# Kernel tuning notes

Measured on AMD Instinct MI355X. Metric: run time of the kernel, lower is better.

Reference implementation:

```python
import jax, jax.numpy as jnp
import numpy as np

B, N, D, H = 16, 2048, 256, 256  # batch, sensor points, branch dim, hidden dim


def setup_inputs() -> dict:
    key = jax.random.key(0)
    ks = jax.random.split(key, 12)
    s = 0.02
    return {
        "x": jax.random.normal(ks[0], (B, N), dtype=jnp.float32),
        "grid": jax.random.uniform(ks[1], (N, 1), dtype=jnp.float32),  # cellcenters_nx
        "W1a": jax.random.normal(ks[2], (2, H), dtype=jnp.float32) * s,
        "b1a": jnp.zeros((H,), dtype=jnp.float32),
        "W1b": jax.random.normal(ks[3], (H, D), dtype=jnp.float32) * s,
        "b1b": jnp.zeros((D,), dtype=jnp.float32),
        "Wqkv": jax.random.normal(ks[4], (D, 3 * D), dtype=jnp.float32) * s,
        "W2a": jax.random.normal(ks[5], (D, H), dtype=jnp.float32) * s,
        "b2a": jnp.zeros((H,), dtype=jnp.float32),
        "W2b": jax.random.normal(ks[6], (H, D), dtype=jnp.float32) * s,
        "b2b": jnp.zeros((D,), dtype=jnp.float32),
    }


def reference(x, grid, W1a, b1a, W1b, b1b, Wqkv, W2a, b2a, W2b, b2b):
    b, n = x.shape
    # x.unsqueeze(-1) concat grid -> [B, N, 2]
    g = jnp.broadcast_to(grid[None, :, :], (b, n, 1))
    h = jnp.concatenate([x[..., None], g], axis=-1)
    # littleFNN Linear1: Linear -> GELU(exact) -> Linear
    h = jax.nn.gelu(h @ W1a + b1a, approximate=False) @ W1b + b1b  # [B, N, D]
    # SelfAttention: single fused qkv projection, no bias
    qkv = h @ Wqkv  # [B, N, 3D]
    q, k, v = jnp.split(qkv, 3, axis=-1)
    scale = jnp.asarray(qkv.shape[-1] // 3, h.dtype) ** -0.5
    scores = jnp.einsum("bid,bjd->bij", q, k) * scale  # [B, N, N]
    attn = jax.nn.softmax(scores, axis=-1)
    o = jnp.einsum("bij,bjd->bid", attn, v)  # [B, N, D]
    # littleFNN Linear2
    o = jax.nn.gelu(o @ W2a + b2a, approximate=False) @ W2b + b2b  # [B, N, D]
    return jnp.mean(o, axis=1)  # [B, D]
```

## Files before the change

### kernel.cpp

```cpp
#include <hip/hip_runtime.h>
#include <hip/hip_bf16.h>
#include <cmath>

typedef __attribute__((ext_vector_type(8))) short short8;
typedef __attribute__((ext_vector_type(4))) float f32x4;

#define MFMA16(a, b, c) __builtin_amdgcn_mfma_f32_16x16x32_bf16((a), (b), (c), 0, 0, 0)

static constexpr int BB = 16, NN = 2048, DD = 256, HH = 256;

__device__ inline unsigned short f2bf(float f) {
    union { float f; unsigned int u; } v; v.f = f;
    unsigned int r = v.u + 0x7fffu + ((v.u >> 16) & 1u);
    return (unsigned short)(r >> 16);
}
__device__ inline float bf2f(unsigned short u) {
    union { unsigned int u; float f; } v; v.u = ((unsigned int)u) << 16;
    return v.f;
}
__device__ inline float gelu_exact(float x) {
    return 0.5f * x * (1.0f + erff(x * 0.7071067811865475f));
}
__device__ inline void gload_lds16(const void* g, void* l) {
    __builtin_amdgcn_global_load_lds(
        (const __attribute__((address_space(1))) unsigned int*)g,
        (__attribute__((address_space(3))) unsigned int*)l, 16, 0, 0);
}
__device__ inline void fence_mem() { asm volatile("" ::: "memory"); }
__device__ inline unsigned int cvtpk_bf16(float lo, float hi) {
    unsigned int r;
    asm("v_cvt_pk_bf16_f32 %0, %1, %2" : "=v"(r) : "v"(lo), "v"(hi));
    return r;
}

__global__ __launch_bounds__(256) void transposeT_k(const float* __restrict__ W1b,
                                                    const float* __restrict__ Wqkv,
                                                    const float* __restrict__ W2a,
                                                    unsigned short* __restrict__ W1bT,
                                                    unsigned short* __restrict__ WqkvT,
                                                    unsigned short* __restrict__ W2aT,
                                                    float* __restrict__ bar) {
    __shared__ float tl[64][65];
    int bid = blockIdx.x;
    int t = threadIdx.x;
    if (bid == 0) {
        f32x4 z = (f32x4){0.f, 0.f, 0.f, 0.f};
#pragma unroll
        for (int i = 0; i < 4; i++) *(f32x4*)(bar + t * 16 + i * 4) = z;
    }
    const float* src;
    unsigned short* dst;
    int N, tn, tk;
    if (bid < 16) {
        src = W1b; dst = W1bT; N = 256; tn = bid & 3; tk = bid >> 2;
    } else if (bid < 64) {
        int t2 = bid - 16;
        src = Wqkv; dst = WqkvT; N = 768; tn = t2 % 12; tk = t2 / 12;
    } else {
        int t2 = bid - 64;
        src = W2a; dst = W2aT; N = 256; tn = t2 & 3; tk = t2 >> 2;
    }
    int n0 = tn * 64, k0 = tk * 64;
#pragma unroll
    for (int j = 0; j < 4; j++) {
        int row = (t >> 4) * 4 + j;
        f32x4 v = *(const f32x4*)(src + (size_t)(k0 + row) * N + n0 + (t & 15) * 4);
#pragma unroll
        for (int e = 0; e < 4; e++) tl[row][(t & 15) * 4 + e] = v[e];
    }
    __syncthreads();
    int n = t >> 2, cb = (t & 3) * 16;
    short8 a, b;
#pragma unroll
    for (int e = 0; e < 8; e++) {
        a[e] = (short)f2bf(tl[cb + e][n]);
        b[e] = (short)f2bf(tl[cb + 8 + e][n]);
    }
    *(short8*)(dst + (size_t)(n0 + n) * 256 + k0 + cb) = a;
    *(short8*)(dst + (size_t)(n0 + n) * 256 + k0 + cb + 8) = b;
}

__global__ __launch_bounds__(512) void ffn_qkv_k(const float* __restrict__ x,
                                                 const float* __restrict__ grd,
                                                 const float* __restrict__ W1a,
                                                 const float* __restrict__ b1a,
                                                 const unsigned short* __restrict__ W1bT,
                                                 const float* __restrict__ b1b,
                                                 const unsigned short* __restrict__ WqkvT,
                                                 unsigned short* __restrict__ qo,
                                                 unsigned short* __restrict__ ko,
                                                 unsigned short* __restrict__ vo) {
    __shared__ __attribute__((aligned(16))) char bstage[2][32768];
    __shared__ unsigned short h_lds[4][16 * 256];
    const int w = threadIdx.x >> 6, lane = threadIdx.x & 63;
    const int c = lane & 15, g = lane >> 4;
    const int qsub = w >> 1, nh = w & 1;
    const int rb = blockIdx.x * 64 + qsub * 16;
    const int bb = (blockIdx.x * 64) >> 11;
    const int rowinb = (rb & (NN - 1)) + c;

    const int p0r = rb + c;
    const float xv = x[p0r];
    const float gv = grd[p0r & (NN - 1)];
    short8 tf[8];
#pragma unroll
    for (int kc = 0; kc < 8; kc++) {
        int j0 = kc * 32 + g * 8;
#pragma unroll
        for (int e = 0; e < 8; e += 4) {
            f32x4 wa = *(const f32x4*)(W1a + j0 + e);
            f32x4 wb = *(const f32x4*)(W1a + 256 + j0 + e);
            f32x4 ba = *(const f32x4*)(b1a + j0 + e);
#pragma unroll
            for (int q = 0; q < 4; q++) {
                float v = xv * wa[q] + gv * wb[q] + ba[q];
                tf[kc][e + q] = (short)f2bf(gelu_exact(v));
            }
        }
    }

    const char* Bb0 = (const char*)W1bT;
    const char* Bb1 = (const char*)WqkvT;
    const char* Bb2 = (const char*)WqkvT + 256 * 512;
    const char* Bb3 = (const char*)WqkvT + 512 * 512;

#define STAGE_B(buf_, Bb_, kcp_) do {                                                    \
        _Pragma("unroll")                                                                \
        for (int i_ = 0; i_ < 4; i_++) {                                                 \
            int d_ = i_ * 8192 + w * 1024 + lane * 16;                                   \
            int row_ = d_ >> 7, sl_ = (d_ >> 4) & 7;                                     \
            gload_lds16(Bb_ + (size_t)row_ * 512 + (kcp_) * 128 +                        \
                            ((sl_ ^ (row_ & 7)) << 4),                                   \
                        &bstage[buf_][0] + d_);                                          \
        }                                                                                \
    } while (0)

    short8 hf[8];
#pragma unroll
    for (int kc = 0; kc < 8; kc++) hf[kc] = tf[kc];

    STAGE_B(0, Bb0, 0);

#pragma unroll
    for (int p = 0; p < 4; p++) {
        f32x4 acc[8];
#pragma unroll
        for (int n = 0; n < 8; n++) acc[n] = (f32x4){0.f, 0.f, 0.f, 0.f};

#pragma unroll
        for (int kcp = 0; kcp < 4; kcp++) {
            const int gi = p * 4 + kcp;
            if (gi + 1 < 16) {
                const int ni = gi + 1;
                const char* nb = (ni >> 2) == 0 ? Bb0 : (ni >> 2) == 1 ? Bb1
                                : (ni >> 2) == 2 ? Bb2 : Bb3;
                STAGE_B(ni & 1, nb, ni & 3);
                asm volatile("s_waitcnt vmcnt(4)" ::: "memory");
            } else {
                asm volatile("s_waitcnt vmcnt(0)" ::: "memory");
            }
            __builtin_amdgcn_s_barrier();
            fence_mem();

            const char* bl = &bstage[gi & 1][0];
#pragma unroll
            for (int sub = 0; sub < 2; sub++) {
                short8 a = (p == 0) ? tf[kcp * 2 + sub] : hf[kcp * 2 + sub];
#pragma unroll
                for (int n = 0; n < 8; n++) {
                    int addr = (nh * 128 + n * 16 + c) * 128 +
                               ((((sub << 2) | g) ^ (c & 7)) << 4);
                    short8 bfr = *(const short8*)(bl + addr);
                    if (p == 3) acc[n] = MFMA16(bfr, a, acc[n]);
                    else        acc[n] = MFMA16(a, bfr, acc[n]);
                }
            }
            fence_mem();
            __builtin_amdgcn_s_barrier();
            fence_mem();
        }

        if (p == 0) {
            unsigned short* hl = &h_lds[qsub][0];
#pragma unroll
            for (int n = 0; n < 8; n++) {
                int col = nh * 128 + n * 16 + c;
                float bv = b1b[col];
#pragma unroll
                for (int r = 0; r < 4; r++) {
                    int row = g * 4 + r;
                    hl[row * 256 + (col ^ ((row & 7) << 3))] = f2bf(acc[n][r] + bv);
                }
            }
            __syncthreads();
#pragma unroll
            for (int kc = 0; kc < 8; kc++) {
                hf[kc] = *(const short8*)(hl + c * 256 + ((kc * 32 + g * 8) ^ ((c & 7) << 3)));
            }
        } else if (p == 1) {
#pragma unroll
            for (int n = 0; n < 8; n++)
#pragma unroll
                for (int r = 0; r < 4; r++)
                    qo[(size_t)(rb + g * 4 + r) * 256 + nh * 128 + n * 16 + c] =
                        f2bf(acc[n][r] * (0.0625f * 1.4426950408889634f));
        } else if (p == 2) {
#pragma unroll
            for (int n = 0; n < 8; n++)
#pragma unroll
                for (int r = 0; r < 4; r++)
                    ko[(size_t)(rb + g * 4 + r) * 256 + nh * 128 + n * 16 + c] =
                        f2bf(acc[n][r]);
        } else {
#pragma unroll
            for (int m = 0; m < 8; m++) {
#pragma unroll
                for (int r = 0; r < 4; r++) {
                    int dcol = nh * 128 + m * 16 + g * 4 + r;
                    vo[((size_t)(bb * 256 + dcol)) * NN + rowinb] = f2bf(acc[m][r]);
                }
            }
        }
    }
#undef STAGE_B
}

__global__ __launch_bounds__(512) void attn_k(const unsigned short* __restrict__ qb,
                                              const unsigned short* __restrict__ kb,
                                              const unsigned short* __restrict__ vTb,
                                              const unsigned short* __restrict__ W2aT,
                                              const float* __restrict__ b2a,
                                              float* __restrict__ bar) {
    __shared__ __attribute__((aligned(16))) char smem[74752];
    char* klds = smem;
    char* vlds = smem + 32768;
    unsigned int* p_lds = (unsigned int*)(smem + 65536);
    float* exm = (float*)(smem + 65536 + 8192);
    float* exl = exm + 128;
    const int tid = threadIdx.x;
    const int w = tid >> 6, lane = tid & 63;
    const int c = lane & 15, g = lane >> 4;
    const int qsub = w & 3, dhalf = w >> 2;
    const int khalf = dhalf;
    const int bid = blockIdx.x;
    const int swz = (bid & 7) * 64 + (bid >> 3);
    const int b = swz >> 5;
    const int qt = swz & 31;
    const int qbase = qt * 64 + qsub * 16;
    constexpr int NT = NN / 64;

    const int sl_sub = lane >> 5;
    const int sl_col = (lane & 31) * 16;
    const int vl_row = lane >> 3;
    const size_t vl_off = (size_t)vl_row * (NN * 2) + (size_t)(((lane & 7) ^ vl_row) << 4);

    const short8* qp = (const short8*)(qb + (size_t)(b * NN + qbase + c) * DD + g * 8);
    short8 qf[8];
#pragma unroll
    for (int kc = 0; kc < 8; kc++) qf[kc] = qp[kc * 4];

    const char* kb_bytes = (const char*)(kb + (size_t)(b * NN) * DD);
    const char* vb_bytes = (const char*)(vTb + (size_t)(b * DD) * NN);
    const int kswz = (c & 7) << 4;
    const int pcs = c & 7;

#define STAGE_K(kt_) do {                                                                \
        const char* gk = kb_bytes + ((size_t)((kt_) * 64 + 8 * w)) * 512;                \
        _Pragma("unroll")                                                                \
        for (int s_ = 0; s_ < 4; s_++) {                                                 \
            int row_lo = 2 * s_ + sl_sub;                                                \
            gload_lds16(gk + (size_t)row_lo * 512 + (sl_col ^ (row_lo << 4)),            \
                        klds + (8 * w + 2 * s_) * 512);                                  \
        }                                                                                \
    } while (0)
#define STAGE_V(kt_) do {                                                                \
        const char* gv = vb_bytes + (size_t)(32 * w) * (NN * 2) + (size_t)(kt_) * 128 + vl_off; \
        _Pragma("unroll")                                                                \
        for (int s_ = 0; s_ < 4; s_++) {                                                 \
            gload_lds16(gv + (size_t)(8 * s_) * (NN * 2),                                \
                        vlds + (32 * w + 8 * s_) * 128);                                 \
        }                                                                                \
    } while (0)

    f32x4 oacc[8];
#pragma unroll
    for (int i = 0; i < 8; i++) oacc[i] = (f32x4){0.f, 0.f, 0.f, 0.f};
    float mrun = -INFINITY;
    float lrun = 0.f;
    unsigned int* plw = p_lds + qsub * 512 + c * 32;

    STAGE_K(0);

    for (int kt = 0; kt < NT; kt++) {
        STAGE_V(kt);
        asm volatile("s_waitcnt vmcnt(4)" ::: "memory");
        __builtin_amdgcn_s_barrier();
        fence_mem();

        const char* klb = klds + (size_t)(khalf * 32) * 512;
        f32x4 s0 = (f32x4){0.f, 0.f, 0.f, 0.f};
        f32x4 s1 = (f32x4){0.f, 0.f, 0.f, 0.f};
        __builtin_amdgcn_s_setprio(1);
#pragma unroll
        for (int kc = 0; kc < 8; kc++) {
            short8 qv = qf[kc];
            int col = (kc * 64 + g * 16) ^ kswz;
            short8 kf0 = *(const short8*)(klb + (size_t)c * 512 + col);
            short8 kf1 = *(const short8*)(klb + (size_t)(c + 16) * 512 + col);
            s0 = MFMA16(kf0, qv, s0);
            s1 = MFMA16(kf1, qv, s1);
        }
        __builtin_amdgcn_s_setprio(0);

        float t0 = fmaxf(fmaxf(s0[0], s0[1]), fmaxf(s0[2], s0[3]));
        float t1 = fmaxf(fmaxf(s1[0], s1[1]), fmaxf(s1[2], s1[3]));
        float tmo = fmaxf(t0, t1);
        tmo = fmaxf(tmo, __shfl_xor(tmo, 16));
        tmo = fmaxf(tmo, __shfl_xor(tmo, 32));
        if (g == 0) exm[w * 16 + c] = tmo;
        fence_mem();
        __builtin_amdgcn_s_barrier();
        fence_mem();
        float tmax = fmaxf(tmo, exm[(w ^ 4) * 16 + c]);

        if (kt + 1 < NT) STAGE_K(kt + 1);

        bool need = tmax > mrun + 8.f;
        if (__any(need)) {
            float mn = fmaxf(mrun, tmax);
            float corr = exp2f(mrun - mn);
#pragma unroll
            for (int r = 0; r < 4; r++) s0[r] = exp2f(s0[r] - mn);
#pragma unroll
            for (int r = 0; r < 4; r++) s1[r] = exp2f(s1[r] - mn);
            lrun = lrun * corr + ((s0[0] + s0[1]) + (s0[2] + s0[3])) +
                   ((s1[0] + s1[1]) + (s1[2] + s1[3]));
            mrun = mn;
#pragma unroll
            for (int r = 0; r < 4; r++) {
                float cr = __shfl(corr, 20 * g + r);
#pragma unroll
                for (int nc = 0; nc < 8; nc++) oacc[nc][r] *= cr;
            }
        } else {
#pragma unroll
            for (int r = 0; r < 4; r++) s0[r] = exp2f(s0[r] - mrun);
#pragma unroll
            for (int r = 0; r < 4; r++) s1[r] = exp2f(s1[r] - mrun);
            lrun += ((s0[0] + s0[1]) + (s0[2] + s0[3])) +
                    ((s1[0] + s1[1]) + (s1[2] + s1[3]));
        }

        {
            int jb0 = khalf * 16 + 2 * g;
            int jb1 = khalf * 16 + 8 + 2 * g;
#pragma unroll
            for (int h = 0; h < 2; h++) {
                int j = jb0 + h;
                plw[(((j >> 2) ^ pcs) << 2) | (j & 3)] = cvtpk_bf16(s0[2 * h], s0[2 * h + 1]);
                j = jb1 + h;
                plw[(((j >> 2) ^ pcs) << 2) | (j & 3)] = cvtpk_bf16(s1[2 * h], s1[2 * h + 1]);
            }
        }
        fence_mem();
        if (kt + 1 < NT) {
            asm volatile("s_waitcnt vmcnt(4)" ::: "memory");
        } else {
            asm volatile("s_waitcnt vmcnt(0)" ::: "memory");
        }
        __builtin_amdgcn_s_barrier();
        fence_mem();

        short8 pf0 = *(const short8*)(plw + ((g ^ pcs) << 2));
        short8 pf1 = *(const short8*)(plw + (((4 + g) ^ pcs) << 2));
        __builtin_amdgcn_s_setprio(1);
#pragma unroll
        for (int nc = 0; nc < 8; nc++) {
            const char* vr = vlds + (size_t)(dhalf * 128 + nc * 16 + c) * 128;
            short8 vf0 = *(const short8*)(vr + ((g ^ pcs) << 4));
            short8 vf1 = *(const short8*)(vr + (((4 + g) ^ pcs) << 4));
            oacc[nc] = MFMA16(pf0, vf0, oacc[nc]);
            oacc[nc] = MFMA16(pf1, vf1, oacc[nc]);
        }
        __builtin_amdgcn_s_setprio(0);

        fence_mem();
        __builtin_amdgcn_s_barrier();
        fence_mem();
    }
#undef STAGE_K
#undef STAGE_V

    float lt = lrun;
    lt += __shfl_xor(lt, 16);
    lt += __shfl_xor(lt, 32);
    if (g == 0) exl[w * 16 + c] = lt;
    fence_mem();
    __builtin_amdgcn_s_barrier();
    fence_mem();
    lt += exl[(w ^ 4) * 16 + c];
    float inv_r[4];
#pragma unroll
    for (int r = 0; r < 4; r++) inv_r[r] = 1.f / __shfl(lt, 20 * g + r);

    unsigned short* ol = (unsigned short*)smem;
#pragma unroll
    for (int r = 0; r < 4; r++) {
        int row = 4 * g + r;
        int swr = (row & 7) << 3;
#pragma unroll
        for (int nc = 0; nc < 8; nc++) {
            int col = dhalf * 128 + nc * 16 + c;
            ol[qsub * 4096 + row * 256 + (col ^ swr)] = f2bf(oacc[nc][r] * inv_r[r]);
        }
    }
    fence_mem();
    __builtin_amdgcn_s_barrier();
    fence_mem();

    {
        const int wcol = w * 32;
        float colsum[2] = {0.f, 0.f};
#pragma unroll
        for (int q2 = 0; q2 < 4; q2++) {
            f32x4 acc2[2];
            acc2[0] = (f32x4){0.f, 0.f, 0.f, 0.f};
            acc2[1] = (f32x4){0.f, 0.f, 0.f, 0.f};
            const unsigned short* oq = ol + q2 * 4096;
            const int swc = (c & 7) << 3;
#pragma unroll
            for (int kc = 0; kc < 8; kc++) {
                short8 a = *(const short8*)(oq + c * 256 + ((kc * 32 + g * 8) ^ swc));
#pragma unroll
                for (int nc = 0; nc < 2; nc++) {
                    short8 bfr = *(const short8*)(W2aT + (size_t)(wcol + nc * 16 + c) * 256 + kc * 32 + g * 8);
                    acc2[nc] = MFMA16(a, bfr, acc2[nc]);
                }
            }
#pragma unroll
            for (int nc = 0; nc < 2; nc++) {
                float bv = b2a[wcol + nc * 16 + c];
                float s2 = 0.f;
#pragma unroll
                for (int r = 0; r < 4; r++) s2 += gelu_exact(acc2[nc][r] + bv);
                colsum[nc] += s2;
            }
        }
#pragma unroll
        for (int nc = 0; nc < 2; nc++) {
            float s2 = colsum[nc];
            s2 += __shfl_xor(s2, 16);
            s2 += __shfl_xor(s2, 32);
            if (g == 0) atomicAdd(&bar[b * 256 + wcol + nc * 16 + c], s2);
        }
    }
}

__global__ void final_k(const float* __restrict__ bar, const float* __restrict__ W2b,
                        const float* __restrict__ b2b, float* __restrict__ out) {
    int b = blockIdx.x, d = threadIdx.x;
    float s = 0.f;
    for (int h = 0; h < HH; h++) s += bar[b * HH + h] * W2b[h * DD + d];
    out[b * DD + d] = b2b[d] + s * (1.f / (float)NN);
}

extern "C" void kernel_launch(void* const* d_in, const int* in_sizes, int n_in,
                              void* d_out, int out_size, void* d_ws, size_t ws_size,
                              hipStream_t stream) {
    (void)in_sizes; (void)n_in; (void)out_size; (void)ws_size;
    const float* x    = (const float*)d_in[0];
    const float* grd  = (const float*)d_in[1];
    const float* W1a  = (const float*)d_in[2];
    const float* b1a  = (const float*)d_in[3];
    const float* W1b  = (const float*)d_in[4];
    const float* b1b  = (const float*)d_in[5];
    const float* Wqkv = (const float*)d_in[6];
    const float* W2a  = (const float*)d_in[7];
    const float* b2a  = (const float*)d_in[8];
    const float* W2b  = (const float*)d_in[9];
    const float* b2b  = (const float*)d_in[10];
    float* out = (float*)d_out;

    char* ws = (char*)d_ws;
    const size_t MB = 1024 * 1024;
    unsigned short* q_buf  = (unsigned short*)(ws + 0);
    unsigned short* k_buf  = (unsigned short*)(ws + 16 * MB);
    unsigned short* vT_buf = (unsigned short*)(ws + 32 * MB);
    unsigned short* W1bT   = (unsigned short*)(ws + 80 * MB);
    unsigned short* WqkvT  = (unsigned short*)(ws + 80 * MB + 512 * 1024);
    unsigned short* W2aT   = (unsigned short*)(ws + 81 * MB);
    float*          bar    = (float*)(ws + 81 * MB + 256 * 1024);

    transposeT_k<<<dim3(80), 256, 0, stream>>>(W1b, Wqkv, W2a, W1bT, WqkvT, W2aT, bar);
    ffn_qkv_k<<<dim3(512), 512, 0, stream>>>(x, grd, W1a, b1a, W1bT, b1b, WqkvT,
                                             q_buf, k_buf, vT_buf);
    attn_k<<<dim3(512), 512, 0, stream>>>(q_buf, k_buf, vT_buf, W2aT, b2a, bar);
    final_k<<<dim3(BB), 256, 0, stream>>>(bar, W2b, b2b, out);
}
```

Before: 196.1 us.

## Halve attention tile to 32 queries x 32 keys with 4-wave blocks

Restructures the flash-attention kernel from 512-thread blocks handling 64 queries with 64-key tiles to 256-thread blocks handling 32 queries with 32-key tiles, doubling the grid to 1024 blocks. LDS use drops from about 73KB to about 35KB. This allows more resident blocks per CU and spreads the work over more blocks. In exchange, each K/V tile staged from global memory is reused by fewer queries, the loop runs twice as many iterations, and each iteration does fewer MFMAs between its barriers.

```diff
diff --git a/kernel.cpp b/kernel.cpp
--- a/kernel.cpp
+++ b/kernel.cpp
@@ -225,34 +225,34 @@
 #undef STAGE_B
 }
 
-__global__ __launch_bounds__(512) void attn_k(const unsigned short* __restrict__ qb,
+__global__ __launch_bounds__(256) void attn_k(const unsigned short* __restrict__ qb,
                                               const unsigned short* __restrict__ kb,
                                               const unsigned short* __restrict__ vTb,
                                               const unsigned short* __restrict__ W2aT,
                                               const float* __restrict__ b2a,
                                               float* __restrict__ bar) {
-    __shared__ __attribute__((aligned(16))) char smem[74752];
+    __shared__ __attribute__((aligned(16))) char smem[35328];
     char* klds = smem;
-    char* vlds = smem + 32768;
-    unsigned int* p_lds = (unsigned int*)(smem + 65536);
-    float* exm = (float*)(smem + 65536 + 8192);
-    float* exl = exm + 128;
+    char* vlds = smem + 16384;
+    unsigned int* p_lds = (unsigned int*)(smem + 32768);
+    float* exm = (float*)(smem + 34816);
+    float* exl = exm + 64;
     const int tid = threadIdx.x;
     const int w = tid >> 6, lane = tid & 63;
     const int c = lane & 15, g = lane >> 4;
-    const int qsub = w & 3, dhalf = w >> 2;
+    const int qsub = w & 1, dhalf = w >> 1;
     const int khalf = dhalf;
     const int bid = blockIdx.x;
-    const int swz = (bid & 7) * 64 + (bid >> 3);
-    const int b = swz >> 5;
-    const int qt = swz & 31;
-    const int qbase = qt * 64 + qsub * 16;
-    constexpr int NT = NN / 64;
+    const int swz = (bid & 7) * 128 + (bid >> 3);
+    const int b = swz >> 6;
+    const int qt = swz & 63;
+    const int qbase = qt * 32 + qsub * 16;
+    constexpr int NT = NN / 32;
 
     const int sl_sub = lane >> 5;
     const int sl_col = (lane & 31) * 16;
-    const int vl_row = lane >> 3;
-    const size_t vl_off = (size_t)vl_row * (NN * 2) + (size_t)(((lane & 7) ^ vl_row) << 4);
+    const int vl_row = lane >> 2;
+    const int vl_col = (((lane & 3) ^ (vl_row & 3)) << 4);
 
     const short8* qp = (const short8*)(qb + (size_t)(b * NN + qbase + c) * DD + g * 8);
     short8 qf[8];
@@ -262,10 +262,10 @@
     const char* kb_bytes = (const char*)(kb + (size_t)(b * NN) * DD);
     const char* vb_bytes = (const char*)(vTb + (size_t)(b * DD) * NN);
     const int kswz = (c & 7) << 4;
-    const int pcs = c & 7;
+    const int pcs = c & 3;
 
 #define STAGE_K(kt_) do {                                                                \
-        const char* gk = kb_bytes + ((size_t)((kt_) * 64 + 8 * w)) * 512;                \
+        const char* gk = kb_bytes + ((size_t)((kt_) * 32 + 8 * w)) * 512;                \
         _Pragma("unroll")                                                                \
         for (int s_ = 0; s_ < 4; s_++) {                                                 \
             int row_lo = 2 * s_ + sl_sub;                                                \
@@ -274,11 +274,12 @@
         }                                                                                \
     } while (0)
 #define STAGE_V(kt_) do {                                                                \
-        const char* gv = vb_bytes + (size_t)(32 * w) * (NN * 2) + (size_t)(kt_) * 128 + vl_off; \
+        const char* gv = vb_bytes + (size_t)(64 * w + vl_row) * (NN * 2) +               \
+                         (size_t)(kt_) * 64 + vl_col;                                    \
         _Pragma("unroll")                                                                \
         for (int s_ = 0; s_ < 4; s_++) {                                                 \
-            gload_lds16(gv + (size_t)(8 * s_) * (NN * 2),                                \
-                        vlds + (32 * w + 8 * s_) * 128);                                 \
+            gload_lds16(gv + (size_t)(16 * s_) * (NN * 2),                               \
+                        vlds + (4 * w + s_) * 1024);                                     \
         }                                                                                \
     } while (0)
 
@@ -287,7 +288,7 @@
     for (int i = 0; i < 8; i++) oacc[i] = (f32x4){0.f, 0.f, 0.f, 0.f};
     float mrun = -INFINITY;
     float lrun = 0.f;
-    unsigned int* plw = p_lds + qsub * 512 + c * 32;
+    unsigned int* plw = p_lds + qsub * 256 + c * 16;
 
     STAGE_K(0);
 
@@ -297,31 +298,24 @@
         __builtin_amdgcn_s_barrier();
         fence_mem();
 
-        const char* klb = klds + (size_t)(khalf * 32) * 512;
         f32x4 s0 = (f32x4){0.f, 0.f, 0.f, 0.f};
-        f32x4 s1 = (f32x4){0.f, 0.f, 0.f, 0.f};
         __builtin_amdgcn_s_setprio(1);
 #pragma unroll
         for (int kc = 0; kc < 8; kc++) {
-            short8 qv = qf[kc];
             int col = (kc * 64 + g * 16) ^ kswz;
-            short8 kf0 = *(const short8*)(klb + (size_t)c * 512 + col);
-            short8 kf1 = *(const short8*)(klb + (size_t)(c + 16) * 512 + col);
-            s0 = MFMA16(kf0, qv, s0);
-            s1 = MFMA16(kf1, qv, s1);
+            short8 kf = *(const short8*)(klds + (size_t)(khalf * 16 + c) * 512 + col);
+            s0 = MFMA16(kf, qf[kc], s0);
         }
         __builtin_amdgcn_s_setprio(0);
 
-        float t0 = fmaxf(fmaxf(s0[0], s0[1]), fmaxf(s0[2], s0[3]));
-        float t1 = fmaxf(fmaxf(s1[0], s1[1]), fmaxf(s1[2], s1[3]));
-        float tmo = fmaxf(t0, t1);
+        float tmo = fmaxf(fmaxf(s0[0], s0[1]), fmaxf(s0[2], s0[3]));
         tmo = fmaxf(tmo, __shfl_xor(tmo, 16));
         tmo = fmaxf(tmo, __shfl_xor(tmo, 32));
         if (g == 0) exm[w * 16 + c] = tmo;
         fence_mem();
         __builtin_amdgcn_s_barrier();
         fence_mem();
-        float tmax = fmaxf(tmo, exm[(w ^ 4) * 16 + c]);
+        float tmax = fmaxf(tmo, exm[(w ^ 2) * 16 + c]);
 
         if (kt + 1 < NT) STAGE_K(kt + 1);
 
@@ -331,10 +325,7 @@
             float corr = exp2f(mrun - mn);
 #pragma unroll
             for (int r = 0; r < 4; r++) s0[r] = exp2f(s0[r] - mn);
-#pragma unroll
-            for (int r = 0; r < 4; r++) s1[r] = exp2f(s1[r] - mn);
-            lrun = lrun * corr + ((s0[0] + s0[1]) + (s0[2] + s0[3])) +
-                   ((s1[0] + s1[1]) + (s1[2] + s1[3]));
+            lrun = lrun * corr + ((s0[0] + s0[1]) + (s0[2] + s0[3]));
             mrun = mn;
 #pragma unroll
             for (int r = 0; r < 4; r++) {
@@ -345,21 +336,15 @@
         } else {
 #pragma unroll
             for (int r = 0; r < 4; r++) s0[r] = exp2f(s0[r] - mrun);
-#pragma unroll
-            for (int r = 0; r < 4; r++) s1[r] = exp2f(s1[r] - mrun);
-            lrun += ((s0[0] + s0[1]) + (s0[2] + s0[3])) +
-                    ((s1[0] + s1[1]) + (s1[2] + s1[3]));
+            lrun += ((s0[0] + s0[1]) + (s0[2] + s0[3]));
         }
 
         {
-            int jb0 = khalf * 16 + 2 * g;
-            int jb1 = khalf * 16 + 8 + 2 * g;
+            int jb = khalf * 8 + 2 * g;
 #pragma unroll
             for (int h = 0; h < 2; h++) {
-                int j = jb0 + h;
+                int j = jb + h;
                 plw[(((j >> 2) ^ pcs) << 2) | (j & 3)] = cvtpk_bf16(s0[2 * h], s0[2 * h + 1]);
-                j = jb1 + h;
-                plw[(((j >> 2) ^ pcs) << 2) | (j & 3)] = cvtpk_bf16(s1[2 * h], s1[2 * h + 1]);
             }
         }
         fence_mem();
@@ -371,16 +356,13 @@
         __builtin_amdgcn_s_barrier();
         fence_mem();
 
-        short8 pf0 = *(const short8*)(plw + ((g ^ pcs) << 2));
-        short8 pf1 = *(const short8*)(plw + (((4 + g) ^ pcs) << 2));
+        short8 pf = *(const short8*)(plw + ((g ^ pcs) << 2));
         __builtin_amdgcn_s_setprio(1);
 #pragma unroll
         for (int nc = 0; nc < 8; nc++) {
-            const char* vr = vlds + (size_t)(dhalf * 128 + nc * 16 + c) * 128;
-            short8 vf0 = *(const short8*)(vr + ((g ^ pcs) << 4));
-            short8 vf1 = *(const short8*)(vr + (((4 + g) ^ pcs) << 4));
-            oacc[nc] = MFMA16(pf0, vf0, oacc[nc]);
-            oacc[nc] = MFMA16(pf1, vf1, oacc[nc]);
+            const char* vr = vlds + (size_t)(dhalf * 128 + nc * 16 + c) * 64;
+            short8 vf = *(const short8*)(vr + ((g ^ pcs) << 4));
+            oacc[nc] = MFMA16(pf, vf, oacc[nc]);
         }
         __builtin_amdgcn_s_setprio(0);
 
@@ -398,7 +380,7 @@
     fence_mem();
     __builtin_amdgcn_s_barrier();
     fence_mem();
-    lt += exl[(w ^ 4) * 16 + c];
+    lt += exl[(w ^ 2) * 16 + c];
     float inv_r[4];
 #pragma unroll
     for (int r = 0; r < 4; r++) inv_r[r] = 1.f / __shfl(lt, 20 * g + r);
@@ -411,7 +393,7 @@
 #pragma unroll
         for (int nc = 0; nc < 8; nc++) {
             int col = dhalf * 128 + nc * 16 + c;
-            ol[qsub * 4096 + row * 256 + (col ^ swr)] = f2bf(oacc[nc][r] * inv_r[r]);
+            ol[(qsub * 16 + row) * 256 + (col ^ swr)] = f2bf(oacc[nc][r] * inv_r[r]);
         }
     }
     fence_mem();
@@ -419,26 +401,26 @@
     fence_mem();
 
     {
-        const int wcol = w * 32;
-        float colsum[2] = {0.f, 0.f};
-#pragma unroll
-        for (int q2 = 0; q2 < 4; q2++) {
-            f32x4 acc2[2];
-            acc2[0] = (f32x4){0.f, 0.f, 0.f, 0.f};
-            acc2[1] = (f32x4){0.f, 0.f, 0.f, 0.f};
-            const unsigned short* oq = ol + q2 * 4096;
+        const int wcol = w * 64;
+        float colsum[4] = {0.f, 0.f, 0.f, 0.f};
+#pragma unroll
+        for (int q2 = 0; q2 < 2; q2++) {
+            f32x4 acc2[4];
+#pragma unroll
+            for (int nc = 0; nc < 4; nc++) acc2[nc] = (f32x4){0.f, 0.f, 0.f, 0.f};
+            const unsigned short* oq = ol + q2 * 16 * 256;
             const int swc = (c & 7) << 3;
 #pragma unroll
             for (int kc = 0; kc < 8; kc++) {
                 short8 a = *(const short8*)(oq + c * 256 + ((kc * 32 + g * 8) ^ swc));
 #pragma unroll
-                for (int nc = 0; nc < 2; nc++) {
+                for (int nc = 0; nc < 4; nc++) {
                     short8 bfr = *(const short8*)(W2aT + (size_t)(wcol + nc * 16 + c) * 256 + kc * 32 + g * 8);
                     acc2[nc] = MFMA16(a, bfr, acc2[nc]);
                 }
             }
 #pragma unroll
-            for (int nc = 0; nc < 2; nc++) {
+            for (int nc = 0; nc < 4; nc++) {
                 float bv = b2a[wcol + nc * 16 + c];
                 float s2 = 0.f;
 #pragma unroll
@@ -447,7 +429,7 @@
             }
         }
 #pragma unroll
-        for (int nc = 0; nc < 2; nc++) {
+        for (int nc = 0; nc < 4; nc++) {
             float s2 = colsum[nc];
             s2 += __shfl_xor(s2, 16);
             s2 += __shfl_xor(s2, 32);
@@ -494,6 +476,6 @@
     transposeT_k<<<dim3(80), 256, 0, stream>>>(W1b, Wqkv, W2a, W1bT, WqkvT, W2aT, bar);
     ffn_qkv_k<<<dim3(512), 512, 0, stream>>>(x, grd, W1a, b1a, W1bT, b1b, WqkvT,
                                              q_buf, k_buf, vT_buf);
-    attn_k<<<dim3(512), 512, 0, stream>>>(q_buf, k_buf, vT_buf, W2aT, b2a, bar);
+    attn_k<<<dim3(1024), 256, 0, stream>>>(q_buf, k_buf, vT_buf, W2aT, b2a, bar);
     final_k<<<dim3(BB), 256, 0, stream>>>(bar, W2b, b2b, out);
 }
```

After: 245.1 us. +25.0%, slower.
